# Performance work log

Measured on AMD Instinct MI355X. Metric: run time of the kernel, lower is better.

The kernel has to match this reference:

```python
import jax, jax.numpy as jnp
import numpy as np

EPS = 1e-5

def _lstm_scan(x, mask, Wih, Whh, bih, bhh):
    # x: [B,T,D], mask: [B,T] float (applied to h and c AFTER each step, like the torch code)
    B, T, _ = x.shape
    H = Whh.shape[1]
    x_t = jnp.swapaxes(x, 0, 1)            # [T,B,D]
    m_t = jnp.swapaxes(mask, 0, 1)[:, :, None]  # [T,B,1]
    bias = bih + bhh
    def step(carry, inp):
        h, c = carry
        xt, mt = inp
        gates = xt @ Wih.T + h @ Whh.T + bias   # [B,4H], torch gate order i,f,g,o
        i, f, g, o = jnp.split(gates, 4, axis=-1)
        c = jax.nn.sigmoid(f) * c + jax.nn.sigmoid(i) * jnp.tanh(g)
        h = jax.nn.sigmoid(o) * jnp.tanh(c)
        h = h * mt
        c = c * mt
        return (h, c), h
    h0 = jnp.zeros((B, H), x.dtype)
    _, ys = jax.lax.scan(step, (h0, h0), (x_t, m_t))
    return jnp.swapaxes(ys, 0, 1)          # [B,T,H]

def _layernorm(x, g, b):
    mu = x.mean(-1, keepdims=True)
    var = ((x - mu) ** 2).mean(-1, keepdims=True)
    return (x - mu) * jax.lax.rsqrt(var + EPS) * g + b

def setup_inputs() -> dict:
    key = jax.random.key(0)
    ks = jax.random.split(key, 18)
    B, T, D, H, C = 64, 512, 256, 512, 1000
    def u(k, shape, fan):
        s = 1.0 / np.sqrt(fan)
        return jax.random.uniform(k, shape, jnp.float32, -s, s)
    x = jax.random.normal(ks[0], (B, T, D), jnp.float32)
    reset_mask = jax.random.randint(ks[1], (B, T), 0, 2).astype(jnp.float32)
    return {
        "x": x, "reset_mask": reset_mask,
        # layer 0 LSTM (torch init: U(-1/sqrt(H), 1/sqrt(H)))
        "Wih0": u(ks[2], (4 * H, D), H), "Whh0": u(ks[3], (4 * H, H), H),
        "bih0": u(ks[4], (4 * H,), H), "bhh0": u(ks[5], (4 * H,), H),
        "g0": jnp.ones((H,), jnp.float32), "beta0": jnp.zeros((H,), jnp.float32),
        # layer 1 LSTM
        "Wih1": u(ks[6], (4 * H, H), H), "Whh1": u(ks[7], (4 * H, H), H),
        "bih1": u(ks[8], (4 * H,), H), "bhh1": u(ks[9], (4 * H,), H),
        "g1": jnp.ones((H,), jnp.float32), "beta1": jnp.zeros((H,), jnp.float32),
        # final classifier
        "fcW": u(ks[10], (C, H), H), "fcb": u(ks[11], (C,), H),
    }

def reference(x, reset_mask, Wih0, Whh0, bih0, bhh0, g0, beta0,
              Wih1, Whh1, bih1, bhh1, g1, beta1, fcW, fcb):
    h = _lstm_scan(x, reset_mask, Wih0, Whh0, bih0, bhh0)
    h = _layernorm(jax.nn.relu(h), g0, beta0)
    h = _lstm_scan(h, reset_mask, Wih1, Whh1, bih1, bhh1)
    h = _layernorm(jax.nn.relu(h), g1, beta1)
    return h[:, -1, :] @ fcW.T + fcb        # [B, num_classes]
```

## Files before the change

kernel.cpp:

```cpp
#include <hip/hip_runtime.h>
#include <stdint.h>

#define BB 64
#define TT 512
#define DD 256
#define HH 512
#define NG 2048
#define BT (BB*TT)
#define NCLS 1000
#define MAXS 16

typedef _Float16 f16;
typedef _Float16 f16x2 __attribute__((ext_vector_type(2)));
typedef _Float16 f16x4 __attribute__((ext_vector_type(4)));
typedef _Float16 f16x8 __attribute__((ext_vector_type(8)));
typedef float f32x4 __attribute__((ext_vector_type(4)));

__device__ const int d_OFF[MAXS] = {0,32768,49152,60096,68288,74880,80384,85120,
                                    89216,92864,96192,99200,101952,104512,106880,109120};

__device__ __forceinline__ float sigf(float x) { return 1.0f / (1.0f + __expf(-x)); }
__device__ __forceinline__ float tanh_(float x) {
  float e = __expf(-2.0f * fabsf(x));
  float r = (1.0f - e) / (1.0f + e);
  return copysignf(r, x);
}
__device__ __forceinline__ f32x4 mfma16(f16x8 a, f16x8 b, f32x4 c) {
  return __builtin_amdgcn_mfma_f32_16x16x32_f16(a, b, c, 0, 0, 0);
}
__device__ __forceinline__ void gload16(const void* g, void* l) {
  __builtin_amdgcn_global_load_lds((const __attribute__((address_space(1))) void*)g,
                                   (__attribute__((address_space(3))) void*)l, 16, 0, 0);
}

#define C0 (NG*DD/4)
#define C1 (C0 + NG*HH/4)
#define C2 (C1 + NG*HH/4)
#define C3 (C2 + NG*HH/4)
#define CX (C3 + BT*DD/4)
__global__ __launch_bounds__(256) void prep_weights(
    const float* __restrict__ Wih0, const float* __restrict__ Whh0,
    const float* __restrict__ Wih1, const float* __restrict__ Whh1,
    const float* __restrict__ x,
    const float* __restrict__ bih0, const float* __restrict__ bhh0,
    const float* __restrict__ bih1, const float* __restrict__ bhh1,
    f16* __restrict__ W16ih0, f16* __restrict__ W16hh0,
    f16* __restrict__ W16ih1, f16* __restrict__ W16hh1,
    f16* __restrict__ AX,
    float* __restrict__ bias0, float* __restrict__ bias1) {
  int gi = blockIdx.x * 256 + threadIdx.x;
  for (int i = gi; i < CX; i += gridDim.x * 256) {
    const float* s; f16* d; int o;
    if (i < C0)      { s = Wih0; d = W16ih0; o = i; }
    else if (i < C1) { s = Whh0; d = W16hh0; o = i - C0; }
    else if (i < C2) { s = Wih1; d = W16ih1; o = i - C1; }
    else if (i < C3) { s = Whh1; d = W16hh1; o = i - C2; }
    else             { s = x;    d = AX;     o = i - C3; }
    float4 v = ((const float4*)s)[o];
    f16x4 h = { (f16)v.x, (f16)v.y, (f16)v.z, (f16)v.w };
    ((f16x4*)d)[o] = h;
  }
  if (gi < NG/2) {
    int j = gi * 2;
    bias0[j]   = bih0[j]   + bhh0[j];
    bias0[j+1] = bih0[j+1] + bhh0[j+1];
    bias1[j]   = bih1[j]   + bhh1[j];
    bias1[j+1] = bih1[j+1] + bhh1[j+1];
  }
}

__global__ __launch_bounds__(512) void build_lists(const float* __restrict__ mask,
    int* __restrict__ counts, int* __restrict__ lists,
    int* __restrict__ tailcnt, int* __restrict__ taillist,
    float* __restrict__ selm) {
  int b = blockIdx.x, t = threadIdx.x;
  __shared__ float sm[512];
  __shared__ int lcnt[MAXS], lbase[MAXS];
  sm[t] = mask[b*TT + t];
  if (t < MAXS) lcnt[t] = 0;
  __syncthreads();
  int run = 0;
  for (int j = 1; j <= MAXS; ++j) {
    if (t - j < 0) break;
    if (sm[t - j] != 0.0f) run++; else break;
  }
  selm[b*TT + t] = (run == 0) ? sm[t] : -1.0f;
  bool tail = (run >= MAXS);
  int slot = -1;
  if (!tail && run > 0) slot = atomicAdd(&lcnt[run], 1);
  __syncthreads();
  if (t < MAXS) lbase[t] = atomicAdd(&counts[t*32], lcnt[t]);
  __syncthreads();
  if (!tail && run > 0) lists[d_OFF[run] + lbase[run] + slot] = b*TT + t;
  unsigned long long bal = __ballot(tail);
  int lane = t & 63, w = t >> 6;
  int wpre = __popcll(bal & ((1ull << lane) - 1ull));
  __shared__ int wsum[8];
  if (lane == 0) wsum[w] = __popcll(bal);
  __syncthreads();
  int base = 0;
  for (int i = 0; i < w; ++i) base += wsum[i];
  if (tail) taillist[b*TT + base + wpre] = t;
  if (t == 0) {
    int tot = 0;
    for (int i = 0; i < 8; ++i) tot += wsum[i];
    tailcnt[b] = tot;
  }
}

__global__ __launch_bounds__(512) void proj_act(const f16* __restrict__ A,
    const f16* __restrict__ W, const float* __restrict__ bias,
    f16* __restrict__ G, f16* __restrict__ HS, f16* __restrict__ CS,
    const float* __restrict__ selm, int K) {
  __shared__ __align__(16) f16 smem[128*64 + 256*64];
  f16* As = smem;
  f16* Bs = smem + 128*64;
  __shared__ float sel[128];
  const int nwg = gridDim.x;
  const int cpx = nwg >> 3;
  const int swz = (blockIdx.x & 7) * cpx + (blockIdx.x >> 3);
  const int m0 = (swz >> 3) * 128;
  const int j0 = (swz & 7) * 64;
  const int tid = threadIdx.x;
  const int lane = tid & 63;
  const int w = tid >> 6;
  if (tid < 128) sel[tid] = selm[m0 + tid];

  const f16* asrc[2];
#pragma unroll
  for (int p = 0; p < 2; ++p) {
    int cid = tid + p*512;
    int r = cid >> 3, c = cid & 7;
    int cs = c ^ (r & 7);
    asrc[p] = A + (size_t)(m0 + r)*K + cs*8;
  }
  const f16* bsrc[4];
#pragma unroll
  for (int p = 0; p < 4; ++p) {
    int cid = tid + p*512;
    int grow = cid >> 3, c = cid & 7;
    int cs = c ^ (grow & 7);
    int wrow = (grow >> 6)*512 + j0 + (grow & 63);
    bsrc[p] = W + (size_t)wrow*K + cs*8;
  }

  const int rg = w >> 2;
  const int jg = w & 3;
  const int cl = lane & 15;
  const int kq = lane >> 4;
  f32x4 acc[4][4] = {};

  for (int k0 = 0; k0 < K; k0 += 64) {
#pragma unroll
    for (int p = 0; p < 2; ++p)
      gload16(asrc[p] + k0, As + (tid + p*512)*8);
#pragma unroll
    for (int p = 0; p < 4; ++p)
      gload16(bsrc[p] + k0, Bs + (tid + p*512)*8);
    __syncthreads();
#pragma unroll
    for (int ks = 0; ks < 2; ++ks) {
      int kc = ks*4 + kq;
      f16x8 af[4], bf[4];
#pragma unroll
      for (int mi = 0; mi < 4; ++mi) {
        int row = rg*64 + mi*16 + cl;
        af[mi] = *(const f16x8*)(As + row*64 + ((kc ^ (row & 7))*8));
      }
#pragma unroll
      for (int g = 0; g < 4; ++g) {
        int brow = g*64 + jg*16 + cl;
        bf[g] = *(const f16x8*)(Bs + brow*64 + ((kc ^ (brow & 7))*8));
      }
#pragma unroll
      for (int mi = 0; mi < 4; ++mi)
#pragma unroll
        for (int g = 0; g < 4; ++g)
          acc[mi][g] = mfma16(af[mi], bf[g], acc[mi][g]);
    }
    __syncthreads();
  }

  const int j = j0 + jg*16 + cl;
#pragma unroll
  for (int g = 0; g < 4; ++g) {
    float bb = bias[g*512 + j];
#pragma unroll
    for (int mi = 0; mi < 4; ++mi)
#pragma unroll
      for (int r = 0; r < 4; ++r)
        acc[mi][g][r] += bb;
  }

  f16* stg = smem;
#pragma unroll
  for (int half = 0; half < 2; ++half) {
    if (rg == half) {
#pragma unroll
      for (int mi = 0; mi < 4; ++mi)
#pragma unroll
        for (int g = 0; g < 4; ++g)
#pragma unroll
          for (int r = 0; r < 4; ++r) {
            int row_l = mi*16 + kq*4 + r;
            stg[row_l*264 + g*64 + jg*16 + cl] = (f16)acc[mi][g][r];
          }
    }
    __syncthreads();
    {
      int row_l = tid >> 3, sl = tid & 7;
      int slot = half*64 + row_l;
      int row = m0 + slot;
      int jj = j0 + sl*8;
      f16x8 vi = *(const f16x8*)(stg + row_l*264 +        sl*8);
      f16x8 vf = *(const f16x8*)(stg + row_l*264 +  64 + sl*8);
      f16x8 vg = *(const f16x8*)(stg + row_l*264 + 128 + sl*8);
      f16x8 vo = *(const f16x8*)(stg + row_l*264 + 192 + sl*8);
      float sm = sel[slot];
      if (sm >= 0.0f) {
        f16x8 hv, cv;
#pragma unroll
        for (int e = 0; e < 8; ++e) {
          float c = sigf((float)vi[e]) * tanh_((float)vg[e]);
          float h = sigf((float)vo[e]) * tanh_(c);
          hv[e] = (f16)(h*sm); cv[e] = (f16)(c*sm);
        }
        *(f16x8*)(HS + (size_t)row*HH + jj) = hv;
        *(f16x8*)(CS + (size_t)row*HH + jj) = cv;
      } else {
        *(f16x8*)(G + (size_t)row*NG +        jj) = vi;
        *(f16x8*)(G + (size_t)row*NG +  512 + jj) = vf;
        *(f16x8*)(G + (size_t)row*NG + 1024 + jj) = vg;
        *(f16x8*)(G + (size_t)row*NG + 1536 + jj) = vo;
      }
    }
    __syncthreads();
  }
}

__global__ __launch_bounds__(512) void lstm_step(const f16* __restrict__ Wh,
    const f16* __restrict__ G, f16* __restrict__ HS, f16* __restrict__ CS,
    const float* __restrict__ mask, const int* __restrict__ counts,
    const int* __restrict__ lists, int s) {
  const int cnt = counts[s*32];
  if (cnt == 0) return;
  const int units = ((cnt + 127) >> 7) * 8;
  const int* lst = lists + d_OFF[s];
  const int tid = threadIdx.x;
  const int lane = tid & 63;
  const int w = tid >> 6;
  __shared__ __align__(16) f16 smem[128*64 + 256*64];
  f16* As = smem;
  f16* Bs = smem + 128*64;
  __shared__ int ridx[128];
  __shared__ float rmk[128];
  const int rg = w >> 2;
  const int jg = w & 3;
  const int cl = lane & 15;
  const int kq = lane >> 4;

  for (int u = blockIdx.x; u < units; u += gridDim.x) {
    const int mbase = (u >> 3) * 128;
    const int j0 = (u & 7) * 64;
    if (tid < 128) {
      int i = mbase + tid;
      int r = (i < cnt) ? lst[i] : -1;
      ridx[tid] = r;
      rmk[tid] = (r >= 0) ? mask[r] : 0.0f;
    }
    __syncthreads();

    const f16* asrc[2];
#pragma unroll
    for (int p = 0; p < 2; ++p) {
      int cid = tid + p*512;
      int r = cid >> 3, c = cid & 7;
      int cs = c ^ (r & 7);
      int rr = ridx[r];
      int sr = (rr >= 1 ? rr : 1) - 1;
      asrc[p] = HS + (size_t)sr*HH + cs*8;
    }
    const f16* bsrc[4];
#pragma unroll
    for (int p = 0; p < 4; ++p) {
      int cid = tid + p*512;
      int grow = cid >> 3, c = cid & 7;
      int cs = c ^ (grow & 7);
      int wrow = (grow >> 6)*512 + j0 + (grow & 63);
      bsrc[p] = Wh + (size_t)wrow*HH + cs*8;
    }

    f32x4 acc[4][4] = {};
    for (int k0 = 0; k0 < HH; k0 += 64) {
#pragma unroll
      for (int p = 0; p < 2; ++p)
        gload16(asrc[p] + k0, As + (tid + p*512)*8);
#pragma unroll
      for (int p = 0; p < 4; ++p)
        gload16(bsrc[p] + k0, Bs + (tid + p*512)*8);
      __syncthreads();
#pragma unroll
      for (int ks = 0; ks < 2; ++ks) {
        int kc = ks*4 + kq;
        f16x8 af[4], bf[4];
#pragma unroll
        for (int mi = 0; mi < 4; ++mi) {
          int row = rg*64 + mi*16 + cl;
          af[mi] = *(const f16x8*)(As + row*64 + ((kc ^ (row & 7))*8));
        }
#pragma unroll
        for (int g = 0; g < 4; ++g) {
          int brow = g*64 + jg*16 + cl;
          bf[g] = *(const f16x8*)(Bs + brow*64 + ((kc ^ (brow & 7))*8));
        }
#pragma unroll
        for (int mi = 0; mi < 4; ++mi)
#pragma unroll
          for (int g = 0; g < 4; ++g)
            acc[mi][g] = mfma16(af[mi], bf[g], acc[mi][g]);
      }
      __syncthreads();
    }

    f16* stg = smem;
#pragma unroll
    for (int half = 0; half < 2; ++half) {
      if (rg == half) {
#pragma unroll
        for (int mi = 0; mi < 4; ++mi)
#pragma unroll
          for (int g = 0; g < 4; ++g)
#pragma unroll
            for (int r = 0; r < 4; ++r) {
              int row_l = mi*16 + kq*4 + r;
              stg[row_l*264 + g*64 + jg*16 + cl] = (f16)acc[mi][g][r];
            }
      }
      __syncthreads();
      {
        int row_l = tid >> 3, sl = tid & 7;
        int slot = half*64 + row_l;
        int row = ridx[slot];
        if (row >= 0) {
          int jj = j0 + sl*8;
          f16x8 ai = *(const f16x8*)(stg + row_l*264 +        sl*8);
          f16x8 af2 = *(const f16x8*)(stg + row_l*264 +  64 + sl*8);
          f16x8 ag = *(const f16x8*)(stg + row_l*264 + 128 + sl*8);
          f16x8 ao = *(const f16x8*)(stg + row_l*264 + 192 + sl*8);
          f16x8 Gi = *(const f16x8*)(G + (size_t)row*NG +        jj);
          f16x8 Gf = *(const f16x8*)(G + (size_t)row*NG +  512 + jj);
          f16x8 Gg = *(const f16x8*)(G + (size_t)row*NG + 1024 + jj);
          f16x8 Go = *(const f16x8*)(G + (size_t)row*NG + 1536 + jj);
          f16x8 cp = *(const f16x8*)(CS + (size_t)(row - 1)*HH + jj);
          float m = rmk[slot];
          f16x8 hv, cv;
#pragma unroll
          for (int e = 0; e < 8; ++e) {
            float gi = (float)ai[e] + (float)Gi[e];
            float gf = (float)af2[e] + (float)Gf[e];
            float gg = (float)ag[e] + (float)Gg[e];
            float go = (float)ao[e] + (float)Go[e];
            float c = sigf(gf)*(float)cp[e] + sigf(gi)*tanh_(gg);
            float h = sigf(go)*tanh_(c);
            hv[e] = (f16)(h*m); cv[e] = (f16)(c*m);
          }
          *(f16x8*)(HS + (size_t)row*HH + jj) = hv;
          *(f16x8*)(CS + (size_t)row*HH + jj) = cv;
        }
      }
      __syncthreads();
    }
  }
}

__global__ __launch_bounds__(512) void lstm_step_thin(const f16* __restrict__ Wh,
    const f16* __restrict__ G, f16* __restrict__ HS, f16* __restrict__ CS,
    const float* __restrict__ mask, const int* __restrict__ counts,
    const int* __restrict__ lists, int s) {
  const int cnt = counts[s*32];
  if (cnt == 0) return;
  const int units = ((cnt + 127) >> 7) * 32;
  const int* lst = lists + d_OFF[s];
  const int tid = threadIdx.x;
  const int lane = tid & 63;
  const int w = tid >> 6;
  __shared__ __align__(16) f16 As[128*64];
  __shared__ __align__(16) f16 Bs[64*64];
  __shared__ int ridx[128];
  __shared__ float rmk[128];
  const int cl = lane & 15;
  const int kq = lane >> 4;
  const int rbase = w * 16;

  for (int u = blockIdx.x; u < units; u += gridDim.x) {
    const int mbase = (u >> 5) * 128;
    const int j0 = (u & 31) * 16;
    if (tid < 128) {
      int i = mbase + tid;
      int r = (i < cnt) ? lst[i] : -1;
      ridx[tid] = r;
      rmk[tid] = (r >= 0) ? mask[r] : 0.0f;
    }
    __syncthreads();

    const f16* asrc[2];
#pragma unroll
    for (int p = 0; p < 2; ++p) {
      int cid = tid + p*512;
      int r = cid >> 3, c = cid & 7;
      int cs = c ^ (r & 7);
      int rr = ridx[r];
      int sr = (rr >= 1 ? rr : 1) - 1;
      asrc[p] = HS + (size_t)sr*HH + cs*8;
    }
    const f16* bsrc;
    {
      int grow = tid >> 3, c = tid & 7;
      int cs = c ^ (grow & 7);
      int wrow = (grow >> 4)*512 + j0 + (grow & 15);
      bsrc = Wh + (size_t)wrow*HH + cs*8;
    }

    f32x4 acc[4] = {};
    for (int k0 = 0; k0 < HH; k0 += 64) {
#pragma unroll
      for (int p = 0; p < 2; ++p)
        gload16(asrc[p] + k0, As + (tid + p*512)*8);
      gload16(bsrc + k0, Bs + tid*8);
      __syncthreads();
#pragma unroll
      for (int ks = 0; ks < 2; ++ks) {
        int kc = ks*4 + kq;
        int arow = rbase + cl;
        f16x8 af = *(const f16x8*)(As + arow*64 + ((kc ^ (arow & 7))*8));
        f16x8 bf[4];
#pragma unroll
        for (int g = 0; g < 4; ++g) {
          int brow = g*16 + cl;
          bf[g] = *(const f16x8*)(Bs + brow*64 + ((kc ^ (brow & 7))*8));
        }
#pragma unroll
        for (int g = 0; g < 4; ++g)
          acc[g] = mfma16(af, bf[g], acc[g]);
      }
      __syncthreads();
    }

    const int j = j0 + cl;
#pragma unroll
    for (int r = 0; r < 4; ++r) {
      int slot = rbase + kq*4 + r;
      int row = ridx[slot];
      if (row >= 0) {
        size_t gb = (size_t)row * NG;
        float gi = acc[0][r] + (float)G[gb + j];
        float gf = acc[1][r] + (float)G[gb + 512 + j];
        float gg = acc[2][r] + (float)G[gb + 1024 + j];
        float go = acc[3][r] + (float)G[gb + 1536 + j];
        float cp = (float)CS[(size_t)(row - 1)*HH + j];
        float c = sigf(gf)*cp + sigf(gi)*tanh_(gg);
        float h = sigf(go)*tanh_(c);
        float m = rmk[slot];
        HS[(size_t)row*HH + j] = (f16)(h*m);
        CS[(size_t)row*HH + j] = (f16)(c*m);
      }
    }
    __syncthreads();
  }
}

__global__ __launch_bounds__(512) void lstm_tail(const f16* __restrict__ Wh,
    const f16* __restrict__ G, f16* __restrict__ HS, f16* __restrict__ CS,
    const float* __restrict__ mask, const int* __restrict__ tailcnt,
    const int* __restrict__ taillist) {
  int b = blockIdx.x;
  int n = tailcnt[b];
  if (n == 0) return;
  int tid = threadIdx.x, lane = tid & 63, w = tid >> 6;
  const int rl = lane >> 3;
  const int kb = (lane & 7) * 8;
  __shared__ __align__(16) f16 hsh[HH];
  __shared__ float gsh[NG];
  for (int i = 0; i < n; ++i) {
    int t = taillist[b*TT + i];
    size_t row = (size_t)b*TT + t;
    if (tid < 256)
      ((uint32_t*)hsh)[tid] = ((const uint32_t*)(HS + (row - 1)*HH))[tid];
    __syncthreads();
    f16x8 hreg[8];
#pragma unroll
    for (int kk = 0; kk < 8; ++kk)
      hreg[kk] = *(const f16x8*)(hsh + kb + kk*64);
#pragma unroll 2
    for (int batch = 0; batch < 32; ++batch) {
      int o = (w*32 + batch)*8 + rl;
      const f16* wrow = Wh + (size_t)o*HH + kb;
      float p = 0.0f;
#pragma unroll
      for (int kk = 0; kk < 8; ++kk) {
        f16x8 wv = *(const f16x8*)(wrow + kk*64);
        f16x2 w0 = {wv[0], wv[1]}, w1 = {wv[2], wv[3]}, w2 = {wv[4], wv[5]}, w3 = {wv[6], wv[7]};
        f16x2 h0 = {hreg[kk][0], hreg[kk][1]}, h1 = {hreg[kk][2], hreg[kk][3]},
              h2 = {hreg[kk][4], hreg[kk][5]}, h3 = {hreg[kk][6], hreg[kk][7]};
        p = __builtin_amdgcn_fdot2(w0, h0, p, false);
        p = __builtin_amdgcn_fdot2(w1, h1, p, false);
        p = __builtin_amdgcn_fdot2(w2, h2, p, false);
        p = __builtin_amdgcn_fdot2(w3, h3, p, false);
      }
      p += __shfl_xor(p, 1);
      p += __shfl_xor(p, 2);
      p += __shfl_xor(p, 4);
      if ((lane & 7) == 0) gsh[o] = p + (float)G[row*NG + o];
    }
    __syncthreads();
    {
      float cp = (float)CS[(row - 1)*HH + tid];
      float c = sigf(gsh[512 + tid])*cp + sigf(gsh[tid])*tanh_(gsh[1024 + tid]);
      float h = sigf(gsh[1536 + tid])*tanh_(c);
      float m = mask[row];
      HS[row*HH + tid] = (f16)(h*m);
      CS[row*HH + tid] = (f16)(c*m);
    }
    __syncthreads();
  }
}

__global__ __launch_bounds__(512) void ln_relu(const f16* __restrict__ in,
    const float* __restrict__ g, const float* __restrict__ be,
    f16* __restrict__ out) {
  int lane = threadIdx.x & 63, w = threadIdx.x >> 6;
  int row = blockIdx.x * 8 + w;
  f16x8 hv = *(const f16x8*)(in + (size_t)row*HH + lane*8);
  float xv[8]; float s1 = 0.f, s2 = 0.f;
#pragma unroll
  for (int e = 0; e < 8; ++e) { float x = fmaxf((float)hv[e], 0.f); xv[e] = x; s1 += x; s2 += x*x; }
#pragma unroll
  for (int o = 1; o < 64; o <<= 1) { s1 += __shfl_xor(s1, o); s2 += __shfl_xor(s2, o); }
  float mu = s1 * (1.0f/512.0f);
  float var = s2 * (1.0f/512.0f) - mu*mu;
  float rs = rsqrtf(var + 1e-5f);
  f16x8 ov;
#pragma unroll
  for (int e = 0; e < 8; ++e) ov[e] = (f16)((xv[e] - mu)*rs*g[lane*8+e] + be[lane*8+e]);
  *(f16x8*)(out + (size_t)row*HH + lane*8) = ov;
}

__global__ __launch_bounds__(512) void ln_last(const f16* __restrict__ HS,
    const float* __restrict__ g, const float* __restrict__ be, float* __restrict__ out) {
  int b = blockIdx.x;
  int j = threadIdx.x;
  float x = fmaxf((float)HS[((size_t)b*TT + (TT-1))*HH + j], 0.0f);
  float s1 = x, s2 = x*x;
  for (int o = 32; o > 0; o >>= 1) { s1 += __shfl_down(s1, o); s2 += __shfl_down(s2, o); }
  __shared__ float a1[8], a2[8];
  int w = j >> 6;
  if ((j & 63) == 0) { a1[w] = s1; a2[w] = s2; }
  __syncthreads();
  if (j == 0) {
    float t1 = 0.f, t2 = 0.f;
    for (int i = 0; i < 8; ++i) { t1 += a1[i]; t2 += a2[i]; }
    a1[0] = t1; a2[0] = t2;
  }
  __syncthreads();
  float mu = a1[0] * (1.0f/512.0f);
  float var = a2[0] * (1.0f/512.0f) - mu*mu;
  float y = (x - mu) * rsqrtf(var + 1e-5f) * g[j] + be[j];
  out[b*HH + j] = y;
}

__global__ __launch_bounds__(256) void fc_kernel(const float* __restrict__ hf,
    const float* __restrict__ W, const float* __restrict__ bias, float* __restrict__ out) {
  int b = blockIdx.y;
  int c = blockIdx.x * 256 + threadIdx.x;
  __shared__ float hsh[512];
  hsh[threadIdx.x] = hf[b*HH + threadIdx.x];
  hsh[threadIdx.x + 256] = hf[b*HH + 256 + threadIdx.x];
  __syncthreads();
  if (c < NCLS) {
    const float4* wr = (const float4*)(W + (size_t)c*HH);
    float acc = bias[c];
#pragma unroll 4
    for (int k4 = 0; k4 < 128; ++k4) {
      float4 wv = wr[k4];
      acc += wv.x*hsh[k4*4] + wv.y*hsh[k4*4+1] + wv.z*hsh[k4*4+2] + wv.w*hsh[k4*4+3];
    }
    out[b*NCLS + c] = acc;
  }
}

extern "C" void kernel_launch(void* const* d_in, const int* in_sizes, int n_in,
                              void* d_out, int out_size, void* d_ws, size_t ws_size,
                              hipStream_t stream) {
  (void)in_sizes; (void)n_in; (void)out_size;
  const float* x    = (const float*)d_in[0];
  const float* mask = (const float*)d_in[1];
  const float* Wih0 = (const float*)d_in[2];
  const float* Whh0 = (const float*)d_in[3];
  const float* bih0 = (const float*)d_in[4];
  const float* bhh0 = (const float*)d_in[5];
  const float* g0   = (const float*)d_in[6];
  const float* be0  = (const float*)d_in[7];
  const float* Wih1 = (const float*)d_in[8];
  const float* Whh1 = (const float*)d_in[9];
  const float* bih1 = (const float*)d_in[10];
  const float* bhh1 = (const float*)d_in[11];
  const float* g1   = (const float*)d_in[12];
  const float* be1  = (const float*)d_in[13];
  const float* fcW  = (const float*)d_in[14];
  const float* fcb  = (const float*)d_in[15];
  float* out = (float*)d_out;

  char* ws = (char*)d_ws;
  size_t off = 0;
  auto alloc = [&](size_t bytes) { size_t o = off; off += (bytes + 255) & ~(size_t)255; return o; };
  f16* G      = (f16*)(ws + alloc((size_t)BT*NG*2));
  f16* HS     = (f16*)(ws + alloc((size_t)BT*HH*2));
  f16* CS     = (f16*)(ws + alloc((size_t)BT*HH*2));
  f16* H0LN   = (f16*)(ws + alloc((size_t)BT*HH*2));
  f16* W16ih0 = (f16*)(ws + alloc((size_t)NG*DD*2));
  f16* W16hh0 = (f16*)(ws + alloc((size_t)NG*HH*2));
  f16* W16ih1 = (f16*)(ws + alloc((size_t)NG*HH*2));
  f16* W16hh1 = (f16*)(ws + alloc((size_t)NG*HH*2));
  float* bias0 = (float*)(ws + alloc(NG*4));
  float* bias1 = (float*)(ws + alloc(NG*4));
  int* counts  = (int*)(ws + alloc(4096));
  int* tailcnt = counts + 512;
  int* lists   = (int*)(ws + alloc(111168*4));
  int* taillist= (int*)(ws + alloc((size_t)BT*4));
  float* selm  = (float*)(ws + alloc((size_t)BT*4));
  float* hf    = (float*)(ws + alloc((size_t)BB*HH*4));
  if (ws_size < off) return;

  f16* AX = H0LN;

  hipMemsetAsync(counts, 0, 4096, stream);
  prep_weights<<<dim3(512), dim3(256), 0, stream>>>(Wih0, Whh0, Wih1, Whh1, x,
      bih0, bhh0, bih1, bhh1, W16ih0, W16hh0, W16ih1, W16hh1, AX, bias0, bias1);
  build_lists<<<dim3(BB), dim3(512), 0, stream>>>(mask, counts, lists, tailcnt, taillist, selm);

  for (int layer = 0; layer < 2; ++layer) {
    const f16* Wih16 = layer ? W16ih1 : W16ih0;
    const f16* Whh16 = layer ? W16hh1 : W16hh0;
    const float* bias = layer ? bias1 : bias0;
    const f16* Ain = layer ? H0LN : AX;
    int K = layer ? HH : DD;
    proj_act<<<dim3((BT/128)*8), dim3(512), 0, stream>>>(Ain, Wih16, bias, G, HS, CS, selm, K);
    for (int s = 1; s < 5; ++s)
      lstm_step<<<dim3(512), dim3(512), 0, stream>>>(Whh16, G, HS, CS, mask, counts, lists, s);
    for (int s = 5; s < MAXS; ++s)
      lstm_step_thin<<<dim3(256), dim3(512), 0, stream>>>(Whh16, G, HS, CS, mask, counts, lists, s);
    lstm_tail<<<dim3(BB), dim3(512), 0, stream>>>(Whh16, G, HS, CS, mask, tailcnt, taillist);
    if (layer == 0)
      ln_relu<<<dim3(BT/8), dim3(512), 0, stream>>>(HS, g0, be0, H0LN);
  }

  ln_last<<<dim3(BB), dim3(512), 0, stream>>>(HS, g1, be1, hf);
  fc_kernel<<<dim3(4, BB), dim3(256), 0, stream>>>(hf, fcW, fcb, out);
}
```

Baseline: 804.0 us.

## Load MFMA operands directly from global in thin LSTM steps; fuse head kernels

The thin recurrent step kernel drops its LDS staging and barriers and has each lane read its A and B MFMA fragments straight from global memory. The new kernel also takes over steps 3–4 from the tiled kernel, so it is used for more steps. The final layernorm and the classifier are merged into a single kernel, which removes one launch and the intermediate buffer. The trade-off is uncoalesced fragment loads and no reuse of weights through LDS, which may raise L2 traffic.

```diff
diff --git a/kernel.cpp b/kernel.cpp
--- a/kernel.cpp
+++ b/kernel.cpp
@@ -373,7 +373,7 @@
   }
 }
 
-__global__ __launch_bounds__(512) void lstm_step_thin(const f16* __restrict__ Wh,
+__global__ __launch_bounds__(512) void lstm_step_direct(const f16* __restrict__ Wh,
     const f16* __restrict__ G, f16* __restrict__ HS, f16* __restrict__ CS,
     const float* __restrict__ mask, const int* __restrict__ counts,
     const int* __restrict__ lists, int s) {
@@ -384,8 +384,6 @@
   const int tid = threadIdx.x;
   const int lane = tid & 63;
   const int w = tid >> 6;
-  __shared__ __align__(16) f16 As[128*64];
-  __shared__ __align__(16) f16 Bs[64*64];
   __shared__ int ridx[128];
   __shared__ float rmk[128];
   const int cl = lane & 15;
@@ -403,47 +401,25 @@
     }
     __syncthreads();
 
-    const f16* asrc[2];
-#pragma unroll
-    for (int p = 0; p < 2; ++p) {
-      int cid = tid + p*512;
-      int r = cid >> 3, c = cid & 7;
-      int cs = c ^ (r & 7);
-      int rr = ridx[r];
-      int sr = (rr >= 1 ? rr : 1) - 1;
-      asrc[p] = HS + (size_t)sr*HH + cs*8;
-    }
-    const f16* bsrc;
-    {
-      int grow = tid >> 3, c = tid & 7;
-      int cs = c ^ (grow & 7);
-      int wrow = (grow >> 4)*512 + j0 + (grow & 15);
-      bsrc = Wh + (size_t)wrow*HH + cs*8;
-    }
+    int rr = ridx[rbase + cl];
+    const f16* aptr = HS + (size_t)((rr >= 1 ? rr : 1) - 1)*HH + kq*8;
+    const f16* bp0 = Wh + (size_t)(        j0 + cl)*HH + kq*8;
+    const f16* bp1 = Wh + (size_t)( 512 + j0 + cl)*HH + kq*8;
+    const f16* bp2 = Wh + (size_t)(1024 + j0 + cl)*HH + kq*8;
+    const f16* bp3 = Wh + (size_t)(1536 + j0 + cl)*HH + kq*8;
 
     f32x4 acc[4] = {};
-    for (int k0 = 0; k0 < HH; k0 += 64) {
-#pragma unroll
-      for (int p = 0; p < 2; ++p)
-        gload16(asrc[p] + k0, As + (tid + p*512)*8);
-      gload16(bsrc + k0, Bs + tid*8);
-      __syncthreads();
-#pragma unroll
-      for (int ks = 0; ks < 2; ++ks) {
-        int kc = ks*4 + kq;
-        int arow = rbase + cl;
-        f16x8 af = *(const f16x8*)(As + arow*64 + ((kc ^ (arow & 7))*8));
-        f16x8 bf[4];
-#pragma unroll
-        for (int g = 0; g < 4; ++g) {
-          int brow = g*16 + cl;
-          bf[g] = *(const f16x8*)(Bs + brow*64 + ((kc ^ (brow & 7))*8));
-        }
-#pragma unroll
-        for (int g = 0; g < 4; ++g)
-          acc[g] = mfma16(af, bf[g], acc[g]);
-      }
-      __syncthreads();
+#pragma unroll 4
+    for (int ks = 0; ks < 16; ++ks) {
+      f16x8 af = *(const f16x8*)(aptr + ks*32);
+      f16x8 b0 = *(const f16x8*)(bp0 + ks*32);
+      f16x8 b1 = *(const f16x8*)(bp1 + ks*32);
+      f16x8 b2 = *(const f16x8*)(bp2 + ks*32);
+      f16x8 b3 = *(const f16x8*)(bp3 + ks*32);
+      acc[0] = mfma16(af, b0, acc[0]);
+      acc[1] = mfma16(af, b1, acc[1]);
+      acc[2] = mfma16(af, b2, acc[2]);
+      acc[3] = mfma16(af, b3, acc[3]);
     }
 
     const int j = j0 + cl;
@@ -545,10 +521,12 @@
   *(f16x8*)(out + (size_t)row*HH + lane*8) = ov;
 }
 
-__global__ __launch_bounds__(512) void ln_last(const f16* __restrict__ HS,
-    const float* __restrict__ g, const float* __restrict__ be, float* __restrict__ out) {
+__global__ __launch_bounds__(512) void head_fused(const f16* __restrict__ HS,
+    const float* __restrict__ g, const float* __restrict__ be,
+    const float* __restrict__ W, const float* __restrict__ bias, float* __restrict__ out) {
   int b = blockIdx.x;
   int j = threadIdx.x;
+  __shared__ float hsh[512];
   float x = fmaxf((float)HS[((size_t)b*TT + (TT-1))*HH + j], 0.0f);
   float s1 = x, s2 = x*x;
   for (int o = 32; o > 0; o >>= 1) { s1 += __shfl_down(s1, o); s2 += __shfl_down(s2, o); }
@@ -564,27 +542,21 @@
   __syncthreads();
   float mu = a1[0] * (1.0f/512.0f);
   float var = a2[0] * (1.0f/512.0f) - mu*mu;
-  float y = (x - mu) * rsqrtf(var + 1e-5f) * g[j] + be[j];
-  out[b*HH + j] = y;
-}
-
-__global__ __launch_bounds__(256) void fc_kernel(const float* __restrict__ hf,
-    const float* __restrict__ W, const float* __restrict__ bias, float* __restrict__ out) {
-  int b = blockIdx.y;
-  int c = blockIdx.x * 256 + threadIdx.x;
-  __shared__ float hsh[512];
-  hsh[threadIdx.x] = hf[b*HH + threadIdx.x];
-  hsh[threadIdx.x + 256] = hf[b*HH + 256 + threadIdx.x];
+  hsh[j] = (x - mu) * rsqrtf(var + 1e-5f) * g[j] + be[j];
   __syncthreads();
-  if (c < NCLS) {
-    const float4* wr = (const float4*)(W + (size_t)c*HH);
-    float acc = bias[c];
+#pragma unroll
+  for (int rep = 0; rep < 2; ++rep) {
+    int c = j + rep*512;
+    if (c < NCLS) {
+      const float4* wr = (const float4*)(W + (size_t)c*HH);
+      float acc = bias[c];
 #pragma unroll 4
-    for (int k4 = 0; k4 < 128; ++k4) {
-      float4 wv = wr[k4];
-      acc += wv.x*hsh[k4*4] + wv.y*hsh[k4*4+1] + wv.z*hsh[k4*4+2] + wv.w*hsh[k4*4+3];
-    }
-    out[b*NCLS + c] = acc;
+      for (int k4 = 0; k4 < 128; ++k4) {
+        float4 wv = wr[k4];
+        acc += wv.x*hsh[k4*4] + wv.y*hsh[k4*4+1] + wv.z*hsh[k4*4+2] + wv.w*hsh[k4*4+3];
+      }
+      out[b*NCLS + c] = acc;
+    }
   }
 }
 
@@ -628,7 +600,6 @@
   int* lists   = (int*)(ws + alloc(111168*4));
   int* taillist= (int*)(ws + alloc((size_t)BT*4));
   float* selm  = (float*)(ws + alloc((size_t)BT*4));
-  float* hf    = (float*)(ws + alloc((size_t)BB*HH*4));
   if (ws_size < off) return;
 
   f16* AX = H0LN;
@@ -645,15 +616,14 @@
     const f16* Ain = layer ? H0LN : AX;
     int K = layer ? HH : DD;
     proj_act<<<dim3((BT/128)*8), dim3(512), 0, stream>>>(Ain, Wih16, bias, G, HS, CS, selm, K);
-    for (int s = 1; s < 5; ++s)
+    for (int s = 1; s < 3; ++s)
       lstm_step<<<dim3(512), dim3(512), 0, stream>>>(Whh16, G, HS, CS, mask, counts, lists, s);
-    for (int s = 5; s < MAXS; ++s)
-      lstm_step_thin<<<dim3(256), dim3(512), 0, stream>>>(Whh16, G, HS, CS, mask, counts, lists, s);
+    for (int s = 3; s < MAXS; ++s)
+      lstm_step_direct<<<dim3(256), dim3(512), 0, stream>>>(Whh16, G, HS, CS, mask, counts, lists, s);
     lstm_tail<<<dim3(BB), dim3(512), 0, stream>>>(Whh16, G, HS, CS, mask, tailcnt, taillist);
     if (layer == 0)
       ln_relu<<<dim3(BT/8), dim3(512), 0, stream>>>(HS, g0, be0, H0LN);
   }
 
-  ln_last<<<dim3(BB), dim3(512), 0, stream>>>(HS, g1, be1, hf);
-  fc_kernel<<<dim3(4, BB), dim3(256), 0, stream>>>(hf, fcW, fcb, out);
-}
+  head_fused<<<dim3(BB), dim3(512), 0, stream>>>(HS, g1, be1, fcW, fcb, out);
+}
```

New measurement: 1.195 ms. +48.6%, slower.

## Retile gate GEMMs to 128x128 with 256 threads, shorten step levels, fuse head

Applied to the files above, without the earlier changes.

The input-projection and per-level recurrent GEMM kernels move from a 128x256 tile on 512 threads to a 128x128 tile on 256 threads, with twice as many work units. This aims to improve load balance and occupancy on the small per-level problems, at the cost of more A-tile reloads across units. The number of explicit dependency levels drops from 16 to 10, so more timesteps fall to the tail kernel, which changes how much work goes through the wide kernels. The final layernorm and classifier kernels are fused into one launch, which removes the intermediate buffer and one kernel launch.

```diff
diff --git a/kernel.cpp b/kernel.cpp
--- a/kernel.cpp
+++ b/kernel.cpp
@@ -8,7 +8,7 @@
 #define NG 2048
 #define BT (BB*TT)
 #define NCLS 1000
-#define MAXS 16
+#define MAXS 10
 
 typedef _Float16 f16;
 typedef _Float16 f16x2 __attribute__((ext_vector_type(2)));
@@ -16,8 +16,7 @@
 typedef _Float16 f16x8 __attribute__((ext_vector_type(8)));
 typedef float f32x4 __attribute__((ext_vector_type(4)));
 
-__device__ const int d_OFF[MAXS] = {0,32768,49152,60096,68288,74880,80384,85120,
-                                    89216,92864,96192,99200,101952,104512,106880,109120};
+__device__ const int d_OFF[MAXS] = {0,32768,49152,60096,68288,74880,80384,85120,89216,92864};
 
 __device__ __forceinline__ float sigf(float x) { return 1.0f / (1.0f + __expf(-x)); }
 __device__ __forceinline__ float tanh_(float x) {
@@ -108,55 +107,48 @@
   }
 }
 
-__global__ __launch_bounds__(512) void proj_act(const f16* __restrict__ A,
+__global__ __launch_bounds__(256) void proj_act(const f16* __restrict__ A,
     const f16* __restrict__ W, const float* __restrict__ bias,
     f16* __restrict__ G, f16* __restrict__ HS, f16* __restrict__ CS,
     const float* __restrict__ selm, int K) {
-  __shared__ __align__(16) f16 smem[128*64 + 256*64];
+  __shared__ __align__(16) f16 smem[2*128*64];
   f16* As = smem;
   f16* Bs = smem + 128*64;
   __shared__ float sel[128];
   const int nwg = gridDim.x;
   const int cpx = nwg >> 3;
   const int swz = (blockIdx.x & 7) * cpx + (blockIdx.x >> 3);
-  const int m0 = (swz >> 3) * 128;
-  const int j0 = (swz & 7) * 64;
+  const int m0 = (swz >> 4) * 128;
+  const int j0 = (swz & 15) * 32;
   const int tid = threadIdx.x;
   const int lane = tid & 63;
   const int w = tid >> 6;
   if (tid < 128) sel[tid] = selm[m0 + tid];
 
-  const f16* asrc[2];
-#pragma unroll
-  for (int p = 0; p < 2; ++p) {
-    int cid = tid + p*512;
+  const f16* asrc[4];
+  const f16* bsrc[4];
+#pragma unroll
+  for (int p = 0; p < 4; ++p) {
+    int cid = tid + p*256;
     int r = cid >> 3, c = cid & 7;
     int cs = c ^ (r & 7);
     asrc[p] = A + (size_t)(m0 + r)*K + cs*8;
-  }
-  const f16* bsrc[4];
-#pragma unroll
-  for (int p = 0; p < 4; ++p) {
-    int cid = tid + p*512;
-    int grow = cid >> 3, c = cid & 7;
-    int cs = c ^ (grow & 7);
-    int wrow = (grow >> 6)*512 + j0 + (grow & 63);
+    int wrow = (r >> 5)*512 + j0 + (r & 31);
     bsrc[p] = W + (size_t)wrow*K + cs*8;
   }
 
-  const int rg = w >> 2;
-  const int jg = w & 3;
+  const int wm = (w >> 1) * 64;
+  const int wn = (w & 1) * 64;
   const int cl = lane & 15;
   const int kq = lane >> 4;
   f32x4 acc[4][4] = {};
 
   for (int k0 = 0; k0 < K; k0 += 64) {
 #pragma unroll
-    for (int p = 0; p < 2; ++p)
-      gload16(asrc[p] + k0, As + (tid + p*512)*8);
-#pragma unroll
-    for (int p = 0; p < 4; ++p)
-      gload16(bsrc[p] + k0, Bs + (tid + p*512)*8);
+    for (int p = 0; p < 4; ++p) {
+      gload16(asrc[p] + k0, As + (tid + p*256)*8);
+      gload16(bsrc[p] + k0, Bs + (tid + p*256)*8);
+    }
     __syncthreads();
 #pragma unroll
     for (int ks = 0; ks < 2; ++ks) {
@@ -164,58 +156,59 @@
       f16x8 af[4], bf[4];
 #pragma unroll
       for (int mi = 0; mi < 4; ++mi) {
-        int row = rg*64 + mi*16 + cl;
+        int row = wm + mi*16 + cl;
         af[mi] = *(const f16x8*)(As + row*64 + ((kc ^ (row & 7))*8));
       }
 #pragma unroll
-      for (int g = 0; g < 4; ++g) {
-        int brow = g*64 + jg*16 + cl;
-        bf[g] = *(const f16x8*)(Bs + brow*64 + ((kc ^ (brow & 7))*8));
+      for (int ni = 0; ni < 4; ++ni) {
+        int brow = wn + ni*16 + cl;
+        bf[ni] = *(const f16x8*)(Bs + brow*64 + ((kc ^ (brow & 7))*8));
       }
 #pragma unroll
       for (int mi = 0; mi < 4; ++mi)
 #pragma unroll
-        for (int g = 0; g < 4; ++g)
-          acc[mi][g] = mfma16(af[mi], bf[g], acc[mi][g]);
-    }
-    __syncthreads();
-  }
-
-  const int j = j0 + jg*16 + cl;
-#pragma unroll
-  for (int g = 0; g < 4; ++g) {
-    float bb = bias[g*512 + j];
+        for (int ni = 0; ni < 4; ++ni)
+          acc[mi][ni] = mfma16(af[mi], bf[ni], acc[mi][ni]);
+    }
+    __syncthreads();
+  }
+
+#pragma unroll
+  for (int ni = 0; ni < 4; ++ni) {
+    int c = wn + ni*16 + cl;
+    float bb = bias[(c >> 5)*512 + j0 + (c & 31)];
 #pragma unroll
     for (int mi = 0; mi < 4; ++mi)
 #pragma unroll
       for (int r = 0; r < 4; ++r)
-        acc[mi][g][r] += bb;
+        acc[mi][ni][r] += bb;
   }
 
   f16* stg = smem;
 #pragma unroll
   for (int half = 0; half < 2; ++half) {
-    if (rg == half) {
+    if ((w >> 1) == half) {
 #pragma unroll
       for (int mi = 0; mi < 4; ++mi)
 #pragma unroll
-        for (int g = 0; g < 4; ++g)
+        for (int ni = 0; ni < 4; ++ni)
 #pragma unroll
           for (int r = 0; r < 4; ++r) {
             int row_l = mi*16 + kq*4 + r;
-            stg[row_l*264 + g*64 + jg*16 + cl] = (f16)acc[mi][g][r];
+            stg[row_l*136 + wn + ni*16 + cl] = (f16)acc[mi][ni][r];
           }
     }
     __syncthreads();
     {
-      int row_l = tid >> 3, sl = tid & 7;
+      int row_l = tid >> 2, js = tid & 3;
       int slot = half*64 + row_l;
       int row = m0 + slot;
-      int jj = j0 + sl*8;
-      f16x8 vi = *(const f16x8*)(stg + row_l*264 +        sl*8);
-      f16x8 vf = *(const f16x8*)(stg + row_l*264 +  64 + sl*8);
-      f16x8 vg = *(const f16x8*)(stg + row_l*264 + 128 + sl*8);
-      f16x8 vo = *(const f16x8*)(stg + row_l*264 + 192 + sl*8);
+      int jj = j0 + js*8;
+      const f16* sb = stg + row_l*136 + js*8;
+      f16x8 vi = *(const f16x8*)(sb);
+      f16x8 vf = *(const f16x8*)(sb + 32);
+      f16x8 vg = *(const f16x8*)(sb + 64);
+      f16x8 vo = *(const f16x8*)(sb + 96);
       float sm = sel[slot];
       if (sm >= 0.0f) {
         f16x8 hv, cv;
@@ -238,30 +231,30 @@
   }
 }
 
-__global__ __launch_bounds__(512) void lstm_step(const f16* __restrict__ Wh,
+__global__ __launch_bounds__(256) void lstm_step(const f16* __restrict__ Wh,
     const f16* __restrict__ G, f16* __restrict__ HS, f16* __restrict__ CS,
     const float* __restrict__ mask, const int* __restrict__ counts,
     const int* __restrict__ lists, int s) {
   const int cnt = counts[s*32];
   if (cnt == 0) return;
-  const int units = ((cnt + 127) >> 7) * 8;
+  const int units = ((cnt + 127) >> 7) * 16;
   const int* lst = lists + d_OFF[s];
   const int tid = threadIdx.x;
   const int lane = tid & 63;
   const int w = tid >> 6;
-  __shared__ __align__(16) f16 smem[128*64 + 256*64];
+  __shared__ __align__(16) f16 smem[2*128*64];
   f16* As = smem;
   f16* Bs = smem + 128*64;
   __shared__ int ridx[128];
   __shared__ float rmk[128];
-  const int rg = w >> 2;
-  const int jg = w & 3;
+  const int wm = (w >> 1) * 64;
+  const int wn = (w & 1) * 64;
   const int cl = lane & 15;
   const int kq = lane >> 4;
 
   for (int u = blockIdx.x; u < units; u += gridDim.x) {
-    const int mbase = (u >> 3) * 128;
-    const int j0 = (u & 7) * 64;
+    const int mbase = (u >> 4) * 128;
+    const int j0 = (u & 15) * 32;
     if (tid < 128) {
       int i = mbase + tid;
       int r = (i < cnt) ? lst[i] : -1;
@@ -270,34 +263,27 @@
     }
     __syncthreads();
 
-    const f16* asrc[2];
-#pragma unroll
-    for (int p = 0; p < 2; ++p) {
-      int cid = tid + p*512;
+    const f16* asrc[4];
+    const f16* bsrc[4];
+#pragma unroll
+    for (int p = 0; p < 4; ++p) {
+      int cid = tid + p*256;
       int r = cid >> 3, c = cid & 7;
       int cs = c ^ (r & 7);
       int rr = ridx[r];
       int sr = (rr >= 1 ? rr : 1) - 1;
       asrc[p] = HS + (size_t)sr*HH + cs*8;
-    }
-    const f16* bsrc[4];
-#pragma unroll
-    for (int p = 0; p < 4; ++p) {
-      int cid = tid + p*512;
-      int grow = cid >> 3, c = cid & 7;
-      int cs = c ^ (grow & 7);
-      int wrow = (grow >> 6)*512 + j0 + (grow & 63);
+      int wrow = (r >> 5)*512 + j0 + (r & 31);
       bsrc[p] = Wh + (size_t)wrow*HH + cs*8;
     }
 
     f32x4 acc[4][4] = {};
     for (int k0 = 0; k0 < HH; k0 += 64) {
 #pragma unroll
-      for (int p = 0; p < 2; ++p)
-        gload16(asrc[p] + k0, As + (tid + p*512)*8);
-#pragma unroll
-      for (int p = 0; p < 4; ++p)
-        gload16(bsrc[p] + k0, Bs + (tid + p*512)*8);
+      for (int p = 0; p < 4; ++p) {
+        gload16(asrc[p] + k0, As + (tid + p*256)*8);
+        gload16(bsrc[p] + k0, Bs + (tid + p*256)*8);
+      }
       __syncthreads();
 #pragma unroll
       for (int ks = 0; ks < 2; ++ks) {
@@ -305,19 +291,19 @@
         f16x8 af[4], bf[4];
 #pragma unroll
         for (int mi = 0; mi < 4; ++mi) {
-          int row = rg*64 + mi*16 + cl;
+          int row = wm + mi*16 + cl;
           af[mi] = *(const f16x8*)(As + row*64 + ((kc ^ (row & 7))*8));
         }
 #pragma unroll
-        for (int g = 0; g < 4; ++g) {
-          int brow = g*64 + jg*16 + cl;
-          bf[g] = *(const f16x8*)(Bs + brow*64 + ((kc ^ (brow & 7))*8));
+        for (int ni = 0; ni < 4; ++ni) {
+          int brow = wn + ni*16 + cl;
+          bf[ni] = *(const f16x8*)(Bs + brow*64 + ((kc ^ (brow & 7))*8));
         }
 #pragma unroll
         for (int mi = 0; mi < 4; ++mi)
 #pragma unroll
-          for (int g = 0; g < 4; ++g)
-            acc[mi][g] = mfma16(af[mi], bf[g], acc[mi][g]);
+          for (int ni = 0; ni < 4; ++ni)
+            acc[mi][ni] = mfma16(af[mi], bf[ni], acc[mi][ni]);
       }
       __syncthreads();
     }
@@ -325,28 +311,29 @@
     f16* stg = smem;
 #pragma unroll
     for (int half = 0; half < 2; ++half) {
-      if (rg == half) {
+      if ((w >> 1) == half) {
 #pragma unroll
         for (int mi = 0; mi < 4; ++mi)
 #pragma unroll
-          for (int g = 0; g < 4; ++g)
+          for (int ni = 0; ni < 4; ++ni)
 #pragma unroll
             for (int r = 0; r < 4; ++r) {
               int row_l = mi*16 + kq*4 + r;
-              stg[row_l*264 + g*64 + jg*16 + cl] = (f16)acc[mi][g][r];
+              stg[row_l*136 + wn + ni*16 + cl] = (f16)acc[mi][ni][r];
             }
       }
       __syncthreads();
       {
-        int row_l = tid >> 3, sl = tid & 7;
+        int row_l = tid >> 2, js = tid & 3;
         int slot = half*64 + row_l;
         int row = ridx[slot];
         if (row >= 0) {
-          int jj = j0 + sl*8;
-          f16x8 ai = *(const f16x8*)(stg + row_l*264 +        sl*8);
-          f16x8 af2 = *(const f16x8*)(stg + row_l*264 +  64 + sl*8);
-          f16x8 ag = *(const f16x8*)(stg + row_l*264 + 128 + sl*8);
-          f16x8 ao = *(const f16x8*)(stg + row_l*264 + 192 + sl*8);
+          int jj = j0 + js*8;
+          const f16* sb = stg + row_l*136 + js*8;
+          f16x8 ai  = *(const f16x8*)(sb);
+          f16x8 af2 = *(const f16x8*)(sb + 32);
+          f16x8 ag  = *(const f16x8*)(sb + 64);
+          f16x8 ao  = *(const f16x8*)(sb + 96);
           f16x8 Gi = *(const f16x8*)(G + (size_t)row*NG +        jj);
           f16x8 Gf = *(const f16x8*)(G + (size_t)row*NG +  512 + jj);
           f16x8 Gg = *(const f16x8*)(G + (size_t)row*NG + 1024 + jj);
@@ -545,10 +532,12 @@
   *(f16x8*)(out + (size_t)row*HH + lane*8) = ov;
 }
 
-__global__ __launch_bounds__(512) void ln_last(const f16* __restrict__ HS,
-    const float* __restrict__ g, const float* __restrict__ be, float* __restrict__ out) {
+__global__ __launch_bounds__(512) void head_fused(const f16* __restrict__ HS,
+    const float* __restrict__ g, const float* __restrict__ be,
+    const float* __restrict__ W, const float* __restrict__ bias, float* __restrict__ out) {
   int b = blockIdx.x;
   int j = threadIdx.x;
+  __shared__ float hsh[512];
   float x = fmaxf((float)HS[((size_t)b*TT + (TT-1))*HH + j], 0.0f);
   float s1 = x, s2 = x*x;
   for (int o = 32; o > 0; o >>= 1) { s1 += __shfl_down(s1, o); s2 += __shfl_down(s2, o); }
@@ -564,27 +553,21 @@
   __syncthreads();
   float mu = a1[0] * (1.0f/512.0f);
   float var = a2[0] * (1.0f/512.0f) - mu*mu;
-  float y = (x - mu) * rsqrtf(var + 1e-5f) * g[j] + be[j];
-  out[b*HH + j] = y;
-}
-
-__global__ __launch_bounds__(256) void fc_kernel(const float* __restrict__ hf,
-    const float* __restrict__ W, const float* __restrict__ bias, float* __restrict__ out) {
-  int b = blockIdx.y;
-  int c = blockIdx.x * 256 + threadIdx.x;
-  __shared__ float hsh[512];
-  hsh[threadIdx.x] = hf[b*HH + threadIdx.x];
-  hsh[threadIdx.x + 256] = hf[b*HH + 256 + threadIdx.x];
+  hsh[j] = (x - mu) * rsqrtf(var + 1e-5f) * g[j] + be[j];
   __syncthreads();
-  if (c < NCLS) {
-    const float4* wr = (const float4*)(W + (size_t)c*HH);
-    float acc = bias[c];
+#pragma unroll
+  for (int rep = 0; rep < 2; ++rep) {
+    int c = j + rep*512;
+    if (c < NCLS) {
+      const float4* wr = (const float4*)(W + (size_t)c*HH);
+      float acc = bias[c];
 #pragma unroll 4
-    for (int k4 = 0; k4 < 128; ++k4) {
-      float4 wv = wr[k4];
-      acc += wv.x*hsh[k4*4] + wv.y*hsh[k4*4+1] + wv.z*hsh[k4*4+2] + wv.w*hsh[k4*4+3];
-    }
-    out[b*NCLS + c] = acc;
+      for (int k4 = 0; k4 < 128; ++k4) {
+        float4 wv = wr[k4];
+        acc += wv.x*hsh[k4*4] + wv.y*hsh[k4*4+1] + wv.z*hsh[k4*4+2] + wv.w*hsh[k4*4+3];
+      }
+      out[b*NCLS + c] = acc;
+    }
   }
 }
 
@@ -625,10 +608,9 @@
   float* bias1 = (float*)(ws + alloc(NG*4));
   int* counts  = (int*)(ws + alloc(4096));
   int* tailcnt = counts + 512;
-  int* lists   = (int*)(ws + alloc(111168*4));
+  int* lists   = (int*)(ws + alloc(96192*4));
   int* taillist= (int*)(ws + alloc((size_t)BT*4));
   float* selm  = (float*)(ws + alloc((size_t)BT*4));
-  float* hf    = (float*)(ws + alloc((size_t)BB*HH*4));
   if (ws_size < off) return;
 
   f16* AX = H0LN;
@@ -644,9 +626,9 @@
     const float* bias = layer ? bias1 : bias0;
     const f16* Ain = layer ? H0LN : AX;
     int K = layer ? HH : DD;
-    proj_act<<<dim3((BT/128)*8), dim3(512), 0, stream>>>(Ain, Wih16, bias, G, HS, CS, selm, K);
+    proj_act<<<dim3((BT/128)*16), dim3(256), 0, stream>>>(Ain, Wih16, bias, G, HS, CS, selm, K);
     for (int s = 1; s < 5; ++s)
-      lstm_step<<<dim3(512), dim3(512), 0, stream>>>(Whh16, G, HS, CS, mask, counts, lists, s);
+      lstm_step<<<dim3(1024), dim3(256), 0, stream>>>(Whh16, G, HS, CS, mask, counts, lists, s);
     for (int s = 5; s < MAXS; ++s)
       lstm_step_thin<<<dim3(256), dim3(512), 0, stream>>>(Whh16, G, HS, CS, mask, counts, lists, s);
     lstm_tail<<<dim3(BB), dim3(512), 0, stream>>>(Whh16, G, HS, CS, mask, tailcnt, taillist);
@@ -654,6 +636,5 @@
       ln_relu<<<dim3(BT/8), dim3(512), 0, stream>>>(HS, g0, be0, H0LN);
   }
 
-  ln_last<<<dim3(BB), dim3(512), 0, stream>>>(HS, g1, be1, hf);
-  fc_kernel<<<dim3(4, BB), dim3(256), 0, stream>>>(hf, fcW, fcb, out);
-}
+  head_fused<<<dim3(BB), dim3(512), 0, stream>>>(HS, g1, be1, fcW, fcb, out);
+}
```

Measured after the change: 1.038 ms. +29.1%, slower.
